# Performance work log

Measured on AMD Instinct MI355X. Metric: run time of the kernel, lower is better.

The kernel has to match this reference:

```python
import jax, jax.numpy as jnp
import numpy as np

B, X, Y, T = 8, 256, 256, 64   # input grid; T == fno_width
MODES = 16
PAD = 8
T_LOOKBACK = 16
SCALE = 1.0 / (T * T_LOOKBACK)  # 1/(fno_width*t_lookback)


def setup_inputs() -> dict:
    key = jax.random.key(0)
    ks = jax.random.split(key, 5)
    m = MODES
    x = jax.random.normal(ks[0], (B, X, Y, T), dtype=jnp.float32)
    w_tl = SCALE * jax.random.uniform(ks[1], (m, m, m), dtype=jnp.float32)
    w_tr = SCALE * jax.random.uniform(ks[2], (m, m, m), dtype=jnp.float32)
    w_bl = SCALE * jax.random.uniform(ks[3], (m, m, m), dtype=jnp.float32)
    w_br = SCALE * jax.random.uniform(ks[4], (m, m, m), dtype=jnp.float32)
    z = jnp.zeros((m, m, m), dtype=jnp.float32)
    return {"x": x, "w_tl": w_tl, "w_tr": w_tr, "w_bl": w_bl, "w_br": w_br,
            "b_tl": z, "b_tr": z, "b_bl": z, "b_br": z}


def reference(x, w_tl, w_tr, w_bl, w_br, b_tl, b_tr, b_bl, b_br):
    m, pad = MODES, PAD
    # pad all three non-batch dims
    xp = jnp.pad(x, ((0, 0), (pad, pad), (pad, pad), (pad, pad)))
    # tf: x = complex(x, x); x_ft = real(fft3d(x)) == Re(F(a)) - Im(F(a))
    xc = jax.lax.complex(xp, xp)
    x_ft = jnp.real(jnp.fft.fftn(xc, axes=(1, 2, 3)))
    # four corner mode blocks along axes 1,2; low modes along axis 3
    m_tl = x_ft[:, :m, :m, :m]
    m_tr = x_ft[:, -m:, :m, :m]
    m_bl = x_ft[:, :m, -m:, :m]
    m_br = x_ft[:, -m:, -m:, :m]
    top = jnp.concatenate([m_tl * w_tl + b_tl, m_tr * w_tr + b_tr], axis=1)
    bot = jnp.concatenate([m_bl * w_bl + b_bl, m_br * w_br + b_br], axis=1)
    xwb = jnp.concatenate([top, bot], axis=2)  # [B, 2m, 2m, m]
    # pad back to the UNPADDED input shape (axes 1,2) and to fno_width (axis 3)
    xwb = jnp.pad(xwb, ((0, 0), (0, X - 2 * m), (0, Y - 2 * m), (0, T - m)))
    # tf: output = real(ifft3d(complex(xwb, xwb)))
    out = jnp.real(jnp.fft.ifftn(jax.lax.complex(xwb, xwb), axes=(1, 2, 3)))
    return out
```

## Files before the change

### kernel.cpp

```cpp
#include <hip/hip_runtime.h>

#define PI_D 3.141592653589793238462643383279502884


__global__ void k_tables(float2* __restrict__ wt, float2* __restrict__ vt,
                         float2* __restrict__ vxy,
                         float2* __restrict__ pqf, float2* __restrict__ pqi,
                         float2* __restrict__ t16, float2* __restrict__ t1) {
  int t = blockIdx.x * blockDim.x + threadIdx.x;
  if (t < 64 * 16) {
    int n3 = t >> 4, k3 = t & 15;
    int ph = (k3 * (n3 + 8)) % 80;
    double a = -2.0 * PI_D * (double)ph / 80.0;
    wt[t] = make_float2((float)cos(a), (float)sin(a));
  }
  if (t < 256 * 32) {
    int n = t >> 5, k = t & 31;
    int kk = (k < 16) ? k : (240 + k);
    int ph = (kk * (n + 8)) % 272;
    double a = -2.0 * PI_D * (double)ph / 272.0;
    double c = cos(a), s = sin(a);
    pqf[t] = make_float2((float)(c - s), (float)(-(c + s)));
  }
  if (t < 512) {
    int a = t >> 5, k = t & 31;
    int kk = (k < 16) ? k : (240 + k);
    int ph16 = (kk * 16 * a) % 272;
    double a16 = -2.0 * PI_D * (double)ph16 / 272.0;
    t16[t] = make_float2((float)cos(a16), (float)sin(a16));
    int ph1 = (kk * (a + 8)) % 272;
    double a1 = -2.0 * PI_D * (double)ph1 / 272.0;
    t1[t] = make_float2((float)cos(a1), (float)sin(a1));
  }
  if (t < 16 * 64) {
    int k3 = t >> 6, n3 = t & 63;
    int ph = (k3 * n3) & 63;
    double a = 2.0 * PI_D * (double)ph / 64.0;
    vt[t] = make_float2((float)cos(a), (float)sin(a));
  }
  if (t < 256 * 32) {
    int n = t >> 5, k = t & 31;
    int ph = (k * n) & 255;
    double a = 2.0 * PI_D * (double)ph / 256.0;
    double c = cos(a), s = sin(a);
    vxy[t] = make_float2((float)c, (float)s);
    const double inv = 1.0 / 4194304.0;
    pqi[t] = make_float2((float)((c - s) * inv), (float)((-(c + s)) * inv));
  }
}

__global__ __launch_bounds__(512, 4) void k_fwd(const float* __restrict__ x,
                                                float2* __restrict__ Bm,
                                                const float2* __restrict__ wtf,
                                                const float2* __restrict__ t16,
                                                const float2* __restrict__ t1) {
  __shared__ float sX[32][260];
  __shared__ float sAt[256][36];
  __shared__ float2 swt[1024];
  int bn1 = blockIdx.x;
  int tid = threadIdx.x;
  int lane = tid & 63;
  int wv = __builtin_amdgcn_readfirstlane(tid >> 6);
  int q = wv & 3, hf = wv >> 2;
  int n2a = hf * 128 + 2 * lane;
  const float4* xg = (const float4*)(x + (long)bn1 * 16384);
  swt[tid] = wtf[tid];
  swt[tid + 512] = wtf[tid + 512];
  float2 acc[2][4];
#pragma unroll
  for (int i = 0; i < 2; i++)
#pragma unroll
    for (int k = 0; k < 4; k++) acc[i][k] = make_float2(0.f, 0.f);
  for (int h3 = 0; h3 < 2; h3++) {
    if (h3) __syncthreads();
#pragma unroll
    for (int e = 0; e < 4; e++) {
      int g = tid + e * 512;
      int n2 = g >> 3, q3 = g & 7;
      float4 v = xg[n2 * 16 + h3 * 8 + q3];
      int cs = n2 ^ (q3 * 4);
      sX[4 * q3 + 0][cs] = v.x; sX[4 * q3 + 1][cs] = v.y;
      sX[4 * q3 + 2][cs] = v.z; sX[4 * q3 + 3][cs] = v.w;
    }
    __syncthreads();
#pragma unroll 4
    for (int n3l = 0; n3l < 32; n3l++) {
      float2 xv = *(const float2*)&sX[n3l][n2a ^ ((n3l >> 2) * 4)];
      const float* wr = (const float*)&swt[(h3 * 32 + n3l) * 16 + 4 * q];
      float4 wA = *(const float4*)(wr);
      float4 wB = *(const float4*)(wr + 4);
      acc[0][0].x = fmaf(xv.x, wA.x, acc[0][0].x); acc[0][0].y = fmaf(xv.x, wA.y, acc[0][0].y);
      acc[0][1].x = fmaf(xv.x, wA.z, acc[0][1].x); acc[0][1].y = fmaf(xv.x, wA.w, acc[0][1].y);
      acc[0][2].x = fmaf(xv.x, wB.x, acc[0][2].x); acc[0][2].y = fmaf(xv.x, wB.y, acc[0][2].y);
      acc[0][3].x = fmaf(xv.x, wB.z, acc[0][3].x); acc[0][3].y = fmaf(xv.x, wB.w, acc[0][3].y);
      acc[1][0].x = fmaf(xv.y, wA.x, acc[1][0].x); acc[1][0].y = fmaf(xv.y, wA.y, acc[1][0].y);
      acc[1][1].x = fmaf(xv.y, wA.z, acc[1][1].x); acc[1][1].y = fmaf(xv.y, wA.w, acc[1][1].y);
      acc[1][2].x = fmaf(xv.y, wB.x, acc[1][2].x); acc[1][2].y = fmaf(xv.y, wB.y, acc[1][2].y);
      acc[1][3].x = fmaf(xv.y, wB.z, acc[1][3].x); acc[1][3].y = fmaf(xv.y, wB.w, acc[1][3].y);
    }
  }
#pragma unroll
  for (int i = 0; i < 2; i++) {
    int row = n2a + i;
    *(float4*)&sAt[row][8 * q] =
        make_float4(acc[i][0].x, acc[i][0].y, acc[i][1].x, acc[i][1].y);
    *(float4*)&sAt[row][8 * q + 4] =
        make_float4(acc[i][2].x, acc[i][2].y, acc[i][3].x, acc[i][3].y);
  }
  int k2 = lane & 31, s = lane >> 5;
  float2 W16[16], W1s[8];
#pragma unroll
  for (int a = 0; a < 16; a++) W16[a] = t16[a * 32 + k2];
#pragma unroll
  for (int u = 0; u < 8; u++) W1s[u] = t1[(2 * u + s) * 32 + k2];
  __syncthreads();
  {
    int p = wv;
    float2 a0 = make_float2(0.f, 0.f), a1 = make_float2(0.f, 0.f);
#pragma unroll
    for (int a = 0; a < 16; a++) {
      float2 wa = W16[a];
#pragma unroll
      for (int u = 0; u < 8; u++) {
        int n2 = 16 * a + 2 * u + s;
        float4 av = *(const float4*)&sAt[n2][4 * p];
        float2 wb = W1s[u];
        float wx = fmaf(wa.x, wb.x, -wa.y * wb.y);
        float wy = fmaf(wa.x, wb.y, wa.y * wb.x);
        a0.x = fmaf(av.x, wx, fmaf(-av.y, wy, a0.x));
        a0.y = fmaf(av.x, wy, fmaf(av.y, wx, a0.y));
        a1.x = fmaf(av.z, wx, fmaf(-av.w, wy, a1.x));
        a1.y = fmaf(av.z, wy, fmaf(av.w, wx, a1.y));
      }
    }
    a0.x += __shfl_xor(a0.x, 32); a0.y += __shfl_xor(a0.y, 32);
    a1.x += __shfl_xor(a1.x, 32); a1.y += __shfl_xor(a1.y, 32);
    if (s == 0) {
      *(float4*)&Bm[(long)bn1 * 512 + k2 * 16 + 2 * p] =
          make_float4(a0.x, a0.y, a1.x, a1.y);
    }
  }
}

__global__ __launch_bounds__(512, 2) void k_fft_x(
    const float2* __restrict__ Bm, float* __restrict__ y,
    const float2* __restrict__ pqf,
    const float* __restrict__ w_tl, const float* __restrict__ w_tr,
    const float* __restrict__ w_bl, const float* __restrict__ w_br,
    const float* __restrict__ b_tl, const float* __restrict__ b_tr,
    const float* __restrict__ b_bl, const float* __restrict__ b_br) {
  __shared__ float2 sB[4096];
  __shared__ float2 sPQ[8192];
  int b = blockIdx.x >> 5, k2 = blockIdx.x & 31;
  int tid = threadIdx.x;
  for (int i = tid; i < 4096; i += 512) {
    sB[i] = Bm[((long)(b * 256 + (i >> 4)) * 32 + k2) * 16 + (i & 15)];
  }
  const float4* pq4 = (const float4*)pqf;
  float4* sPQ4 = (float4*)sPQ;
#pragma unroll
  for (int e = 0; e < 8; e++) sPQ4[tid + e * 512] = pq4[tid + e * 512];
  __syncthreads();
  int k1 = tid >> 4, k3 = tid & 15;
  float acc = 0.f;
#pragma unroll 8
  for (int n1 = 0; n1 < 256; n1++) {
    float2 a = sB[n1 * 16 + k3];
    float2 w = sPQ[n1 * 32 + k1];
    acc = fmaf(a.x, w.x, acc);
    acc = fmaf(a.y, w.y, acc);
  }
  const float* wsel = (k1 < 16) ? ((k2 < 16) ? w_tl : w_bl) : ((k2 < 16) ? w_tr : w_br);
  const float* bsel = (k1 < 16) ? ((k2 < 16) ? b_tl : b_bl) : ((k2 < 16) ? b_tr : b_br);
  int idx = ((k1 & 15) * 16 + (k2 & 15)) * 16 + k3;
  y[((b * 32 + k1) * 32 + k2) * 16 + k3] = fmaf(acc, wsel[idx], bsel[idx]);
}

__global__ __launch_bounds__(256, 2) void k_inv_te(const float* __restrict__ y,
                                                   float2* __restrict__ E,
                                                   const float2* __restrict__ vt,
                                                   const float2* __restrict__ vxy) {
  __shared__ float sy[512];
  __shared__ float2 svt[1024];
  __shared__ float sD[32][132];
  __shared__ float sV[128][66];
  int blk = blockIdx.x;
  int h = blk & 1, bk1 = blk >> 1;
  int tid = threadIdx.x;
  ((float2*)sy)[tid] = ((const float2*)(y + (long)bk1 * 512))[tid];
#pragma unroll
  for (int e = 0; e < 4; e++) svt[tid + e * 256] = vt[tid + e * 256];
#pragma unroll
  for (int e = 0; e < 16; e++) {
    int q = tid + e * 256;
    int n2l = q >> 5, k2 = q & 31;
    float2 v = vxy[(h * 128 + n2l) * 32 + k2];
    *(float2*)&sV[n2l][2 * k2] = v;
  }
  __syncthreads();
#pragma unroll
  for (int e = 0; e < 8; e++) {
    int idx = tid + e * 256;
    int k2 = idx >> 6, n3i = idx & 63;
    float ax = 0.f, ay = 0.f;
#pragma unroll
    for (int k3 = 0; k3 < 16; k3++) {
      float yv = sy[k2 * 16 + k3];
      float2 v = svt[k3 * 64 + n3i];
      ax = fmaf(yv, v.x, ax); ay = fmaf(yv, v.y, ay);
    }
    *(float2*)&sD[k2][2 * n3i] = make_float2(ax, ay);
  }
  __syncthreads();
  int rg = tid >> 3, tn = tid & 7;
  float acc[4][16];
#pragma unroll
  for (int i = 0; i < 4; i++)
#pragma unroll
    for (int j = 0; j < 16; j++) acc[i][j] = 0.f;
#pragma unroll 2
  for (int k2 = 0; k2 < 32; k2++) {
    float4 d0 = *(const float4*)&sD[k2][tn * 16];
    float4 d1 = *(const float4*)&sD[k2][tn * 16 + 4];
    float4 d2 = *(const float4*)&sD[k2][tn * 16 + 8];
    float4 d3 = *(const float4*)&sD[k2][tn * 16 + 12];
#pragma unroll
    for (int i = 0; i < 4; i++) {
      float2 v = *(const float2*)&sV[rg * 4 + i][2 * k2];
      float c = v.x, s = v.y;
      acc[i][0]  = fmaf(c, d0.x, fmaf(-s, d0.y, acc[i][0]));
      acc[i][1]  = fmaf(c, d0.y, fmaf( s, d0.x, acc[i][1]));
      acc[i][2]  = fmaf(c, d0.z, fmaf(-s, d0.w, acc[i][2]));
      acc[i][3]  = fmaf(c, d0.w, fmaf( s, d0.z, acc[i][3]));
      acc[i][4]  = fmaf(c, d1.x, fmaf(-s, d1.y, acc[i][4]));
      acc[i][5]  = fmaf(c, d1.y, fmaf( s, d1.x, acc[i][5]));
      acc[i][6]  = fmaf(c, d1.z, fmaf(-s, d1.w, acc[i][6]));
      acc[i][7]  = fmaf(c, d1.w, fmaf( s, d1.z, acc[i][7]));
      acc[i][8]  = fmaf(c, d2.x, fmaf(-s, d2.y, acc[i][8]));
      acc[i][9]  = fmaf(c, d2.y, fmaf( s, d2.x, acc[i][9]));
      acc[i][10] = fmaf(c, d2.z, fmaf(-s, d2.w, acc[i][10]));
      acc[i][11] = fmaf(c, d2.w, fmaf( s, d2.z, acc[i][11]));
      acc[i][12] = fmaf(c, d3.x, fmaf(-s, d3.y, acc[i][12]));
      acc[i][13] = fmaf(c, d3.y, fmaf( s, d3.x, acc[i][13]));
      acc[i][14] = fmaf(c, d3.z, fmaf(-s, d3.w, acc[i][14]));
      acc[i][15] = fmaf(c, d3.w, fmaf( s, d3.z, acc[i][15]));
    }
  }
#pragma unroll
  for (int i = 0; i < 4; i++) {
    int n2g = h * 128 + rg * 4 + i;
    float4* dst = (float4*)&E[((long)bk1 * 256 + n2g) * 64 + tn * 8];
    dst[0] = make_float4(acc[i][0], acc[i][1], acc[i][2], acc[i][3]);
    dst[1] = make_float4(acc[i][4], acc[i][5], acc[i][6], acc[i][7]);
    dst[2] = make_float4(acc[i][8], acc[i][9], acc[i][10], acc[i][11]);
    dst[3] = make_float4(acc[i][12], acc[i][13], acc[i][14], acc[i][15]);
  }
}

__global__ __launch_bounds__(256, 2) void k_ifft_x(const float2* __restrict__ E,
                                                   float* __restrict__ out,
                                                   const float2* __restrict__ pqi) {
  __shared__ float sW[64][256];
  __shared__ float sD[64][64];
  int blk = blockIdx.x;
  int tc = blk & 255, b = blk >> 8;
  int tid = threadIdx.x;
  {
    const float4* pq4 = (const float4*)pqi;
#pragma unroll
    for (int r = 0; r < 16; r++) {
      float4 v = pq4[tid * 16 + r];
      sW[4 * r][tid] = v.x; sW[4 * r + 1][tid] = v.y;
      sW[4 * r + 2][tid] = v.z; sW[4 * r + 3][tid] = v.w;
    }
  }
  {
    const float4* Eg = (const float4*)E;
#pragma unroll
    for (int e = 0; e < 2; e++) {
      int tq = tid + e * 256;
      int k1 = tq >> 4, cq = tq & 15;
      const float4* src = Eg + ((long)(b * 32 + k1) * 8192) + tc * 32 + 2 * cq;
      float4 v0 = src[0], v1 = src[1];
      *(float4*)&sD[2 * k1][4 * cq]     = make_float4(v0.x, v0.z, v1.x, v1.z);
      *(float4*)&sD[2 * k1 + 1][4 * cq] = make_float4(v0.y, v0.w, v1.y, v1.w);
    }
  }
  __syncthreads();
  int tm = tid >> 3, tn = tid & 7;
  float acc[8][8];
#pragma unroll
  for (int i = 0; i < 8; i++)
#pragma unroll
    for (int j = 0; j < 8; j++) acc[i][j] = 0.f;
#pragma unroll 2
  for (int kk = 0; kk < 64; kk++) {
    float4 wa = *(const float4*)&sW[kk][tm * 8];
    float4 wb = *(const float4*)&sW[kk][tm * 8 + 4];
    float4 da = *(const float4*)&sD[kk][tn * 8];
    float4 db = *(const float4*)&sD[kk][tn * 8 + 4];
    float w[8] = {wa.x, wa.y, wa.z, wa.w, wb.x, wb.y, wb.z, wb.w};
    float d[8] = {da.x, da.y, da.z, da.w, db.x, db.y, db.z, db.w};
#pragma unroll
    for (int i = 0; i < 8; i++)
#pragma unroll
      for (int j = 0; j < 8; j++) acc[i][j] = fmaf(w[i], d[j], acc[i][j]);
  }
  float* ob = out + (long)b * 4194304 + (long)(tm * 8) * 16384 + tc * 64 + tn * 8;
#pragma unroll
  for (int i = 0; i < 8; i++) {
    float4* o = (float4*)(ob + (long)i * 16384);
    o[0] = make_float4(acc[i][0], acc[i][1], acc[i][2], acc[i][3]);
    o[1] = make_float4(acc[i][4], acc[i][5], acc[i][6], acc[i][7]);
  }
}

extern "C" void kernel_launch(void* const* d_in, const int* in_sizes, int n_in,
                              void* d_out, int out_size, void* d_ws, size_t ws_size,
                              hipStream_t stream) {
  const float* x    = (const float*)d_in[0];
  const float* w_tl = (const float*)d_in[1];
  const float* w_tr = (const float*)d_in[2];
  const float* w_bl = (const float*)d_in[3];
  const float* w_br = (const float*)d_in[4];
  const float* b_tl = (const float*)d_in[5];
  const float* b_tr = (const float*)d_in[6];
  const float* b_bl = (const float*)d_in[7];
  const float* b_br = (const float*)d_in[8];
  float* out = (float*)d_out;
  char* ws = (char*)d_ws;

  float2* Bm  = (float2*)(ws + 0);
  float*  y   = (float*)(ws + 8388608);
  float2* E   = (float2*)(ws + 10485760);
  float2* WT  = (float2*)(ws + 44040192);
  float2* VT  = (float2*)(ws + 44048384);
  float2* VXY = (float2*)(ws + 44056576);
  float2* PQF = (float2*)(ws + 44122112);
  float2* PQI = (float2*)(ws + 44187648);
  float2* T16 = (float2*)(ws + 44253184);
  float2* T1  = (float2*)(ws + 44257280);

  k_tables<<<32, 256, 0, stream>>>(WT, VT, VXY, PQF, PQI, T16, T1);
  k_fwd<<<2048, 512, 0, stream>>>(x, Bm, WT, T16, T1);
  k_fft_x<<<256, 512, 0, stream>>>(Bm, y, PQF, w_tl, w_tr, w_bl, w_br,
                                   b_tl, b_tr, b_bl, b_br);
  k_inv_te<<<512, 256, 0, stream>>>(y, E, VT, VXY);
  k_ifft_x<<<2048, 256, 0, stream>>>(E, out, PQI);
}
```

Measured before the change: 189.5 us.

## Restructure k_fwd T-axis DFT: per-wave mode split, global twiddles, smaller tiles

Reworks the first-stage DFT along the time axis in k_fwd. Each wave now owns 2 output modes and each lane handles 4 consecutive n2 rows, instead of 8 modes per wave over 2 rows. The input is staged in four 16-deep chunks instead of two 32-deep ones, which shrinks the sX tile. Twiddles are read straight from global memory (wave-uniform, so likely scalar or cached loads) instead of being copied into LDS, and the launch bound rises to 6 blocks per CU. This cuts LDS footprint and LDS twiddle traffic to raise occupancy, at the cost of more barriers and repeated global twiddle reads.

```diff
diff --git a/kernel.cpp b/kernel.cpp
--- a/kernel.cpp
+++ b/kernel.cpp
@@ -49,63 +49,55 @@
   }
 }
 
-__global__ __launch_bounds__(512, 4) void k_fwd(const float* __restrict__ x,
+__global__ __launch_bounds__(512, 6) void k_fwd(const float* __restrict__ x,
                                                 float2* __restrict__ Bm,
-                                                const float2* __restrict__ wtf,
+                                                const float* __restrict__ wtf,
                                                 const float2* __restrict__ t16,
                                                 const float2* __restrict__ t1) {
-  __shared__ float sX[32][260];
+  __shared__ float sX[16][260];
   __shared__ float sAt[256][36];
-  __shared__ float2 swt[1024];
   int bn1 = blockIdx.x;
   int tid = threadIdx.x;
   int lane = tid & 63;
-  int wv = __builtin_amdgcn_readfirstlane(tid >> 6);
-  int q = wv & 3, hf = wv >> 2;
-  int n2a = hf * 128 + 2 * lane;
+  int p = __builtin_amdgcn_readfirstlane(tid >> 6);
   const float4* xg = (const float4*)(x + (long)bn1 * 16384);
-  swt[tid] = wtf[tid];
-  swt[tid + 512] = wtf[tid + 512];
-  float2 acc[2][4];
-#pragma unroll
-  for (int i = 0; i < 2; i++)
-#pragma unroll
-    for (int k = 0; k < 4; k++) acc[i][k] = make_float2(0.f, 0.f);
-  for (int h3 = 0; h3 < 2; h3++) {
-    if (h3) __syncthreads();
-#pragma unroll
-    for (int e = 0; e < 4; e++) {
-      int g = tid + e * 512;
-      int n2 = g >> 3, q3 = g & 7;
-      float4 v = xg[n2 * 16 + h3 * 8 + q3];
-      int cs = n2 ^ (q3 * 4);
-      sX[4 * q3 + 0][cs] = v.x; sX[4 * q3 + 1][cs] = v.y;
-      sX[4 * q3 + 2][cs] = v.z; sX[4 * q3 + 3][cs] = v.w;
+  const float* wrow = wtf + 4 * p;
+  float2 acc[4][2];
+#pragma unroll
+  for (int i = 0; i < 4; i++) {
+    acc[i][0] = make_float2(0.f, 0.f);
+    acc[i][1] = make_float2(0.f, 0.f);
+  }
+  for (int Q = 0; Q < 4; Q++) {
+    if (Q) __syncthreads();
+#pragma unroll
+    for (int e = 0; e < 2; e++) {
+      int idx = tid + e * 512;
+      int n2 = idx >> 2, qq = idx & 3;
+      float4 v = xg[n2 * 16 + 4 * Q + qq];
+      int cs = n2 ^ (qq * 4);
+      sX[4 * qq + 0][cs] = v.x; sX[4 * qq + 1][cs] = v.y;
+      sX[4 * qq + 2][cs] = v.z; sX[4 * qq + 3][cs] = v.w;
     }
     __syncthreads();
-#pragma unroll 4
-    for (int n3l = 0; n3l < 32; n3l++) {
-      float2 xv = *(const float2*)&sX[n3l][n2a ^ ((n3l >> 2) * 4)];
-      const float* wr = (const float*)&swt[(h3 * 32 + n3l) * 16 + 4 * q];
-      float4 wA = *(const float4*)(wr);
-      float4 wB = *(const float4*)(wr + 4);
-      acc[0][0].x = fmaf(xv.x, wA.x, acc[0][0].x); acc[0][0].y = fmaf(xv.x, wA.y, acc[0][0].y);
-      acc[0][1].x = fmaf(xv.x, wA.z, acc[0][1].x); acc[0][1].y = fmaf(xv.x, wA.w, acc[0][1].y);
-      acc[0][2].x = fmaf(xv.x, wB.x, acc[0][2].x); acc[0][2].y = fmaf(xv.x, wB.y, acc[0][2].y);
-      acc[0][3].x = fmaf(xv.x, wB.z, acc[0][3].x); acc[0][3].y = fmaf(xv.x, wB.w, acc[0][3].y);
-      acc[1][0].x = fmaf(xv.y, wA.x, acc[1][0].x); acc[1][0].y = fmaf(xv.y, wA.y, acc[1][0].y);
-      acc[1][1].x = fmaf(xv.y, wA.z, acc[1][1].x); acc[1][1].y = fmaf(xv.y, wA.w, acc[1][1].y);
-      acc[1][2].x = fmaf(xv.y, wB.x, acc[1][2].x); acc[1][2].y = fmaf(xv.y, wB.y, acc[1][2].y);
-      acc[1][3].x = fmaf(xv.y, wB.z, acc[1][3].x); acc[1][3].y = fmaf(xv.y, wB.w, acc[1][3].y);
-    }
-  }
-#pragma unroll
-  for (int i = 0; i < 2; i++) {
-    int row = n2a + i;
-    *(float4*)&sAt[row][8 * q] =
+#pragma unroll
+    for (int n3l = 0; n3l < 16; n3l++) {
+      float4 xv = *(const float4*)&sX[n3l][(4 * lane) ^ ((n3l >> 2) * 4)];
+      float4 w = *(const float4*)(wrow + (16 * Q + n3l) * 32);
+      acc[0][0].x = fmaf(xv.x, w.x, acc[0][0].x); acc[0][0].y = fmaf(xv.x, w.y, acc[0][0].y);
+      acc[0][1].x = fmaf(xv.x, w.z, acc[0][1].x); acc[0][1].y = fmaf(xv.x, w.w, acc[0][1].y);
+      acc[1][0].x = fmaf(xv.y, w.x, acc[1][0].x); acc[1][0].y = fmaf(xv.y, w.y, acc[1][0].y);
+      acc[1][1].x = fmaf(xv.y, w.z, acc[1][1].x); acc[1][1].y = fmaf(xv.y, w.w, acc[1][1].y);
+      acc[2][0].x = fmaf(xv.z, w.x, acc[2][0].x); acc[2][0].y = fmaf(xv.z, w.y, acc[2][0].y);
+      acc[2][1].x = fmaf(xv.z, w.z, acc[2][1].x); acc[2][1].y = fmaf(xv.z, w.w, acc[2][1].y);
+      acc[3][0].x = fmaf(xv.w, w.x, acc[3][0].x); acc[3][0].y = fmaf(xv.w, w.y, acc[3][0].y);
+      acc[3][1].x = fmaf(xv.w, w.z, acc[3][1].x); acc[3][1].y = fmaf(xv.w, w.w, acc[3][1].y);
+    }
+  }
+#pragma unroll
+  for (int i = 0; i < 4; i++) {
+    *(float4*)&sAt[4 * lane + i][4 * p] =
         make_float4(acc[i][0].x, acc[i][0].y, acc[i][1].x, acc[i][1].y);
-    *(float4*)&sAt[row][8 * q + 4] =
-        make_float4(acc[i][2].x, acc[i][2].y, acc[i][3].x, acc[i][3].y);
   }
   int k2 = lane & 31, s = lane >> 5;
   float2 W16[16], W1s[8];
@@ -115,7 +107,6 @@
   for (int u = 0; u < 8; u++) W1s[u] = t1[(2 * u + s) * 32 + k2];
   __syncthreads();
   {
-    int p = wv;
     float2 a0 = make_float2(0.f, 0.f), a1 = make_float2(0.f, 0.f);
 #pragma unroll
     for (int a = 0; a < 16; a++) {
@@ -342,7 +333,7 @@
   float2* T1  = (float2*)(ws + 44257280);
 
   k_tables<<<32, 256, 0, stream>>>(WT, VT, VXY, PQF, PQI, T16, T1);
-  k_fwd<<<2048, 512, 0, stream>>>(x, Bm, WT, T16, T1);
+  k_fwd<<<2048, 512, 0, stream>>>(x, Bm, (const float*)WT, T16, T1);
   k_fft_x<<<256, 512, 0, stream>>>(Bm, y, PQF, w_tl, w_tr, w_bl, w_br,
                                    b_tl, b_tr, b_bl, b_br);
   k_inv_te<<<512, 256, 0, stream>>>(y, E, VT, VXY);
```

New measurement: 186.4 us. Within noise of the previous version (-1.7%).
